# Performance work log

Hardware: AMD Instinct MI355X
Metric: run time of the kernel (lower is better)

## Reference

```python
import jax, jax.numpy as jnp
import numpy as np


def fps(xyz, npoint):
    # xyz: [B, N, 3] -> idx [B, npoint]; iterative farthest point sampling (start at index 0)
    B, N, _ = xyz.shape
    dist0 = jnp.full((B, N), 1e10, xyz.dtype)
    far0 = jnp.zeros((B,), jnp.int32)
    def body(carry, _):
        dist, far = carry
        centroid = jnp.take_along_axis(xyz, far[:, None, None], axis=1)  # [B,1,3]
        d = jnp.sum((xyz - centroid) ** 2, axis=-1)                      # [B,N]
        dist = jnp.minimum(dist, d)
        return (dist, jnp.argmax(dist, axis=-1).astype(jnp.int32)), far
    _, idx = jax.lax.scan(body, (dist0, far0), None, length=npoint)
    return idx.T  # [B, npoint]


def ball_query(radius, nsample, xyz, new_xyz):
    # xyz [B,N,3], new_xyz [B,S,3] -> idx [B,S,nsample]
    B, S, _ = new_xyz.shape
    N = xyz.shape[1]
    sqr = jnp.sum((new_xyz[:, :, None, :] - xyz[:, None, :, :]) ** 2, axis=-1)  # [B,S,N]
    idx = jnp.broadcast_to(jnp.arange(N, dtype=jnp.int32), (B, S, N))
    idx = jnp.where(sqr > radius * radius, N, idx)
    idx = jnp.sort(idx, axis=-1)[:, :, :nsample]
    first = idx[:, :, :1]
    return jnp.where(idx == N, first, idx)


def index_points(points, idx):
    # points [B,N,C], idx [B,...] int -> [B,...,C]
    B = points.shape[0]
    out = jnp.take_along_axis(points, idx.reshape(B, -1, 1), axis=1)
    return out.reshape(idx.shape + (points.shape[-1],))


def set_abstraction(xyz, points, npoint, radius, nsample, ws, bs):
    fidx = fps(xyz, npoint)
    new_xyz = index_points(xyz, fidx)                       # [B,S,3]
    gidx = ball_query(radius, nsample, xyz, new_xyz)        # [B,S,ns]
    grouped = index_points(xyz, gidx) - new_xyz[:, :, None, :]  # centered neighbors
    if points is not None:
        grouped = jnp.concatenate([grouped, index_points(points, gidx)], axis=-1)
    x = grouped                                             # [B,S,ns,Cin]
    for w, b in zip(ws, bs):  # shared 1x1-conv MLP (eval-mode BN folded into w,b) + ReLU
        x = jax.nn.relu(jnp.einsum('bsnc,oc->bsno', x, w) + b)
    return new_xyz, jnp.max(x, axis=2)                      # max-pool over neighbors


def sa_group_all(xyz, points, ws, bs):
    x = jnp.concatenate([xyz, points], axis=-1)             # [B,N,3+C]
    for w, b in zip(ws, bs):
        x = jax.nn.relu(jnp.einsum('bnc,oc->bno', x, w) + b)
    return jnp.max(x, axis=1)                               # [B,1024]


def setup_inputs() -> dict:
    key = jax.random.key(0)
    ks = iter(jax.random.split(key, 64))
    def w(shape):
        return jax.random.normal(next(ks), shape, jnp.float32) * 0.02
    d = {"xyz": jax.random.normal(next(ks), (32, 3, 4096), jnp.float32)}
    mlps = {"s1": [(64, 3), (64, 64), (128, 64)],
            "s2": [(128, 131), (128, 128), (256, 128)],
            "s3": [(256, 259), (512, 256), (1024, 512)]}
    for name, layers in mlps.items():
        for i, (o, c) in enumerate(layers):
            d[name + "w" + str(i)] = w((o, c))
            d[name + "b" + str(i)] = jnp.zeros((o,), jnp.float32)
    for name, (o, c) in {"f1": (512, 1024), "f2": (256, 512), "f3": (6, 256)}.items():
        d[name + "w"] = w((o, c))
        d[name + "b"] = jnp.zeros((o,), jnp.float32)
    return d


def reference(xyz, s1w0, s1b0, s1w1, s1b1, s1w2, s1b2,
              s2w0, s2b0, s2w1, s2b1, s2w2, s2b2,
              s3w0, s3b0, s3w1, s3b1, s3w2, s3b2,
              f1w, f1b, f2w, f2b, f3w, f3b):
    pts = jnp.transpose(xyz, (0, 2, 1))  # [B,N,3]
    l1x, l1p = set_abstraction(pts, None, 512, 0.2, 32, [s1w0, s1w1, s1w2], [s1b0, s1b1, s1b2])
    l2x, l2p = set_abstraction(l1x, l1p, 128, 0.4, 64, [s2w0, s2w1, s2w2], [s2b0, s2b1, s2b2])
    feat = sa_group_all(l2x, l2p, [s3w0, s3w1, s3w2], [s3b0, s3b1, s3b2])  # [B,1024]
    x = jax.nn.relu(feat @ f1w.T + f1b)   # fc1 + (folded BN) + ReLU; dropout=identity (eval)
    x = jax.nn.relu(x @ f2w.T + f2b)
    return x @ f3w.T + f3b                # [B,6] value head (softmax=False)
```

## Files before the change

### kernel.cpp

```cpp
#include <hip/hip_runtime.h>
#include <hip/hip_bf16.h>


typedef __attribute__((ext_vector_type(8))) short short8;
typedef __attribute__((ext_vector_type(4))) float f32x4;
union SV8 { short8 v; ushort u[8]; };

__device__ __forceinline__ ushort f2bf(float x) {
    unsigned u = __float_as_uint(x);
    unsigned r = (u + 0x7fffu + ((u >> 16) & 1u)) >> 16;
    return (ushort)r;
}

template<int CTRL>
__device__ __forceinline__ unsigned long long dpp_mov_u64(unsigned long long x) {
    const int lo = (int)(unsigned)(x & 0xffffffffull);
    const int hi = (int)(unsigned)(x >> 32);
    const int nlo = __builtin_amdgcn_update_dpp(lo, lo, CTRL, 0xf, 0xf, false);
    const int nhi = __builtin_amdgcn_update_dpp(hi, hi, CTRL, 0xf, 0xf, false);
    return ((unsigned long long)(unsigned)nhi << 32) | (unsigned)nlo;
}

__device__ __forceinline__ unsigned long long wave_max_u64(unsigned long long x) {
    unsigned long long y;
    y = dpp_mov_u64<0x111>(x); if (y > x) x = y;
    y = dpp_mov_u64<0x112>(x); if (y > x) x = y;
    y = dpp_mov_u64<0x114>(x); if (y > x) x = y;
    y = dpp_mov_u64<0x118>(x); if (y > x) x = y;
    y = dpp_mov_u64<0x142>(x); if (y > x) x = y;
    y = dpp_mov_u64<0x143>(x); if (y > x) x = y;
    return x;
}

template<int N, int S, int NT, bool CHW>
__device__ __forceinline__ void fps_body(const float* __restrict__ xyz,
                                         float* __restrict__ new_xyz,
                                         int b, int t, char* smem) {
    constexpr int P  = N / NT;
    constexpr int NW = NT / 64;
    float4* sxyz = (float4*)smem;
    unsigned long long* rv = (unsigned long long*)(smem + (size_t)N * 16);
    int* sfar = (int*)(smem + (size_t)N * 16 + 2 * NW * 8);
    float px[P], py[P], pz[P], dist[P];
    unsigned idc[P];
    if (CHW) {
        const float* base = xyz + (size_t)b * 3 * N;
        #pragma unroll
        for (int p = 0; p < P; ++p) {
            const int i = p * NT + t;
            px[p] = base[i]; py[p] = base[N + i]; pz[p] = base[2 * N + i];
            sxyz[i] = make_float4(px[p], py[p], pz[p], 0.0f);
        }
    } else {
        const float* base = xyz + (size_t)b * N * 3;
        #pragma unroll
        for (int p = 0; p < P; ++p) {
            const int i = p * NT + t;
            px[p] = base[i*3]; py[p] = base[i*3+1]; pz[p] = base[i*3+2];
            sxyz[i] = make_float4(px[p], py[p], pz[p], 0.0f);
        }
    }
    #pragma unroll
    for (int p = 0; p < P; ++p) { dist[p] = 1e10f; idc[p] = (unsigned)(N - 1 - (p * NT + t)); }
    __syncthreads();
    int far = 0;
    for (int j = 0; j < S; ++j) {
        if (t == 0) sfar[j] = far;
        const float4 cen = sxyz[far];
        unsigned long long pk[P];
        #pragma unroll
        for (int p = 0; p < P; ++p) {
            const float dx = px[p] - cen.x, dy = py[p] - cen.y, dz = pz[p] - cen.z;
            const float d = __fadd_rn(__fadd_rn(__fmul_rn(dx, dx), __fmul_rn(dy, dy)), __fmul_rn(dz, dz));
            const float nd = fminf(dist[p], d);
            dist[p] = nd;
            pk[p] = ((unsigned long long)__float_as_uint(nd) << 32) | idc[p];
        }
        #pragma unroll
        for (int s = P / 2; s > 0; s >>= 1)
            #pragma unroll
            for (int k = 0; k < s; ++k)
                if (pk[k + s] > pk[k]) pk[k] = pk[k + s];
        unsigned long long best = wave_max_u64(pk[0]);
        if constexpr (NW > 1) {
            const int sl = (j & 1) * NW;
            if ((t & 63) == 63) rv[sl + (t >> 6)] = best;
            __syncthreads();
            unsigned long long bb = rv[sl];
            #pragma unroll
            for (int w = 1; w < NW; ++w) { const unsigned long long v = rv[sl + w]; if (v > bb) bb = v; }
            far = N - 1 - (int)(bb & 0xffffffffull);
        } else {
            far = N - 1 - __builtin_amdgcn_readlane((int)(best & 0xffffffffull), 63);
        }
    }
    __syncthreads();
    float* out = new_xyz + (size_t)b * S * 3;
    for (int i = t; i < S; i += NT) {
        const float4 c = sxyz[sfar[i]];
        out[i*3+0] = c.x; out[i*3+1] = c.y; out[i*3+2] = c.z;
    }
}

__device__ __forceinline__ void packg(const float* __restrict__ src,
                                      ushort* __restrict__ dh,
                                      int Ktot, int otiles, int cofs, int idx) {
    const int j = idx & 7, lane = (idx >> 3) & 63;
    const int ot = (idx >> 9) % otiles;
    const int ks = idx / (512 * otiles);
    const int m = lane & 15, q = lane >> 4;
    const int o = ot * 16 + m, c = cofs + ks * 32 + q * 8 + j;
    const float v = (c < Ktot) ? src[(size_t)o * Ktot + c] : 0.0f;
    dh[idx] = f2bf(v);
}

__global__ __launch_bounds__(256)
void fps1_prep_kernel(const float* __restrict__ xyz, float* __restrict__ l1xyz,
                 const float* s1w0, const float* s1b0, float4* Wc1,
                 const float* s1w1, ushort* M1W1h,
                 const float* s1w2, ushort* M1W2h,
                 const float* s3w0, ushort* S3W0h,
                 const float* s3w1, ushort* S3W1h,
                 const float* s3w2, ushort* S3W2h,
                 const float* s2w0, const float* s2b0, float4* Wc0,
                 ushort* W0h,
                 const float* s2w1, ushort* W1h,
                 const float* s2w2, ushort* W2h) {
    __shared__ __align__(16) char smem[4096 * 16 + 64 + 512 * 4];
    if (blockIdx.x < 32) {
        fps_body<4096, 512, 256, true>(xyz, l1xyz, blockIdx.x, threadIdx.x, smem);
        return;
    }
    int i = (blockIdx.x - 32) * 256 + threadIdx.x;
    if (i < 64)     { Wc1[i] = make_float4(s1w0[i*3], s1w0[i*3+1], s1w0[i*3+2], s1b0[i]); return; }  i -= 64;
    if (i < 4096)   { packg(s1w1, M1W1h,  64,  4, 0, i); return; }   i -= 4096;
    if (i < 8192)   { packg(s1w2, M1W2h,  64,  8, 0, i); return; }   i -= 8192;
    if (i < 73728)  { packg(s3w0, S3W0h, 259, 16, 0, i); return; }   i -= 73728;
    if (i < 131072) { packg(s3w1, S3W1h, 256, 32, 0, i); return; }   i -= 131072;
    if (i < 524288) { packg(s3w2, S3W2h, 512, 64, 0, i); return; }   i -= 524288;
    if (i < 16384)  { packg(s2w0, W0h, 131,  8, 3, i); return; }     i -= 16384;
    if (i < 16384)  { packg(s2w1, W1h, 128,  8, 0, i); return; }     i -= 16384;
    if (i < 32768)  { packg(s2w2, W2h, 128, 16, 0, i); return; }     i -= 32768;
    if (i < 128) {
        Wc0[i] = make_float4(s2w0[(size_t)i*131+0], s2w0[(size_t)i*131+1],
                             s2w0[(size_t)i*131+2], s2b0[i]);
    }
}

template<int N, int NS, bool CHW, int NT>
__global__ __launch_bounds__(NT)
void bq_kernel(float r2, const float* __restrict__ xyz, const float* __restrict__ cen,
               int* __restrict__ gidx, int S) {
    constexpr int WPB = NT / 64;
    __shared__ __align__(16) float4 sp[N];
    const int t = threadIdx.x, lane = t & 63, w = t >> 6;
    const int cen0 = blockIdx.x * WPB;
    const int b = cen0 / S;
    if (CHW) {
        const float* base = xyz + (size_t)b * 3 * N;
        for (int i = t; i < N; i += NT)
            sp[i] = make_float4(base[i], base[N + i], base[2 * N + i], 0.0f);
    } else {
        const float* base = xyz + (size_t)b * N * 3;
        for (int i = t; i < N; i += NT)
            sp[i] = make_float4(base[i*3], base[i*3+1], base[i*3+2], 0.0f);
    }
    __syncthreads();
    const int wid = cen0 + w;
    const float cx = cen[(size_t)wid*3+0], cy = cen[(size_t)wid*3+1], cz = cen[(size_t)wid*3+2];
    int* out = gidx + (size_t)wid * NS;
    int cnt = 0, first = -1;
    for (int b0 = 0; b0 < N; b0 += 64) {
        const float4 p = sp[b0 + lane];
        const float dx = p.x - cx, dy = p.y - cy, dz = p.z - cz;
        const float d = __fadd_rn(__fadd_rn(__fmul_rn(dx, dx), __fmul_rn(dy, dy)), __fmul_rn(dz, dz));
        const bool in = (d <= r2);
        const unsigned long long m = __ballot(in);
        if (first < 0 && m != 0ull) first = b0 + __ffsll((unsigned long long)m) - 1;
        const int pos = cnt + (int)__popcll(m & ((1ull << lane) - 1ull));
        if (in && pos < NS) out[pos] = b0 + lane;
        cnt += (int)__popcll(m);
        if (cnt >= NS) break;
    }
    if (cnt < NS)
        for (int k = cnt + lane; k < NS; k += 64) out[k] = first;
}

__global__ __launch_bounds__(256)
void mlp1_kernel(const float* __restrict__ xyz, const float* __restrict__ l1xyz,
                 float* __restrict__ l2xyz,
                 const int* __restrict__ gidx, const float4* __restrict__ Wc1,
                 const ushort* __restrict__ W1h, const float* __restrict__ b1,
                 const ushort* __restrict__ W2h, const float* __restrict__ b2,
                 float* __restrict__ l1p) {
    __shared__ __align__(16) char smem[64 * 68 * 4 * 2];
    float* bufA = (float*)smem;
    float* bufB = (float*)(smem + 64 * 68 * 4);
    const int t = threadIdx.x, b = blockIdx.y;
    if (blockIdx.x == 256) {
        fps_body<512, 128, 256, false>(l1xyz, l2xyz, b, t, smem);
        return;
    }
    const int s0 = blockIdx.x * 2;
    {
        const int n = t >> 2, c = t & 3;
        const int s = s0 + (n >> 5);
        const int gi = gidx[((size_t)b * 512 + s) * 32 + (n & 31)];
        float v = 0.0f;
        if (c < 3) v = xyz[(size_t)b * 3 * 4096 + c * 4096 + gi] - l1xyz[((size_t)b * 512 + s) * 3 + c];
        bufB[n * 4 + c] = v;
    }
    __syncthreads();
    {
        const int o = t & 63, ng = t >> 6;
        const float4 wc = Wc1[o];
        #pragma unroll
        for (int r = 0; r < 16; ++r) {
            const int n = ng * 16 + r;
            const float z = wc.w + wc.x * bufB[n*4] + wc.y * bufB[n*4+1] + wc.z * bufB[n*4+2];
            bufA[n * 68 + o] = fmaxf(z, 0.0f);
        }
    }
    const int lane = t & 63, wv = t >> 6;
    const int m = lane & 15, q = lane >> 4;
    const int rowA = wv * 16 + m;
    f32x4 acc1[4];
    #pragma unroll
    for (int ot = 0; ot < 4; ++ot)
        #pragma unroll
        for (int r = 0; r < 4; ++r) acc1[ot][r] = 0.0f;
    #pragma unroll
    for (int ks = 0; ks < 2; ++ks) {
        float xv[8];
        *(float4*)&xv[0] = *(const float4*)&bufA[rowA * 68 + ks * 32 + q * 8];
        *(float4*)&xv[4] = *(const float4*)&bufA[rowA * 68 + ks * 32 + q * 8 + 4];
        SV8 ah;
        #pragma unroll
        for (int j = 0; j < 8; ++j) ah.u[j] = f2bf(xv[j]);
        #pragma unroll
        for (int ot = 0; ot < 4; ++ot) {
            SV8 bh;
            bh.v = *(const short8*)(W1h + (size_t)((ks * 4 + ot) * 64 + lane) * 8);
            acc1[ot] = __builtin_amdgcn_mfma_f32_16x16x32_bf16(ah.v, bh.v, acc1[ot], 0, 0, 0);
        }
    }
    #pragma unroll
    for (int ot = 0; ot < 4; ++ot) {
        const float bb = b1[ot * 16 + m];
        #pragma unroll
        for (int r = 0; r < 4; ++r)
            bufB[(wv * 16 + q * 4 + r) * 68 + ot * 16 + m] = fmaxf(acc1[ot][r] + bb, 0.0f);
    }
    f32x4 acc2[8];
    #pragma unroll
    for (int ot = 0; ot < 8; ++ot)
        #pragma unroll
        for (int r = 0; r < 4; ++r) acc2[ot][r] = 0.0f;
    #pragma unroll
    for (int ks = 0; ks < 2; ++ks) {
        float xv[8];
        *(float4*)&xv[0] = *(const float4*)&bufB[rowA * 68 + ks * 32 + q * 8];
        *(float4*)&xv[4] = *(const float4*)&bufB[rowA * 68 + ks * 32 + q * 8 + 4];
        SV8 ah;
        #pragma unroll
        for (int j = 0; j < 8; ++j) ah.u[j] = f2bf(xv[j]);
        #pragma unroll
        for (int ot = 0; ot < 8; ++ot) {
            SV8 bh;
            bh.v = *(const short8*)(W2h + (size_t)((ks * 8 + ot) * 64 + lane) * 8);
            acc2[ot] = __builtin_amdgcn_mfma_f32_16x16x32_bf16(ah.v, bh.v, acc2[ot], 0, 0, 0);
        }
    }
    __syncthreads();
    #pragma unroll
    for (int ot = 0; ot < 8; ++ot) {
        const float bb = b2[ot * 16 + m];
        float mx = 0.0f;
        #pragma unroll
        for (int r = 0; r < 4; ++r) mx = fmaxf(mx, acc2[ot][r] + bb);
        bufA[(wv * 4 + q) * 128 + ot * 16 + m] = mx;
    }
    __syncthreads();
    {
        const int half = t >> 7, o = t & 127;
        float v = bufA[(half * 8) * 128 + o];
        #pragma unroll
        for (int rr = 1; rr < 8; ++rr) v = fmaxf(v, bufA[(half * 8 + rr) * 128 + o]);
        l1p[((size_t)b * 512 + s0 + half) * 128 + o] = v;
    }
}

__global__ __launch_bounds__(256)
void mlp2_kernel(const float* __restrict__ l1xyz, const float* __restrict__ l1p,
                 const float* __restrict__ l2xyz, const int* __restrict__ gidx,
                 const ushort* __restrict__ W0h, const float4* __restrict__ Wc0,
                 const ushort* __restrict__ W1h, const float* __restrict__ b1,
                 const ushort* __restrict__ W2h, const float* __restrict__ b2,
                 float* __restrict__ X3) {
    __shared__ __align__(16) float Abuf[64 * 132];
    __shared__ __align__(16) float Bbuf[64 * 132];
    __shared__ int sg[64];
    const int t = threadIdx.x, bs = blockIdx.x, b = bs >> 7;
    if (t < 64) sg[t] = gidx[(size_t)bs * 64 + t];
    if (t < 3)  X3[(size_t)bs * 288 + t] = l2xyz[(size_t)bs * 3 + t];
    if (t >= 64 && t < 93) X3[(size_t)bs * 288 + 259 + (t - 64)] = 0.0f;
    __syncthreads();
    for (int i = t; i < 64 * 32; i += 256) {
        const int n = i >> 5, cc = i & 31;
        *(float4*)&Abuf[n * 132 + cc * 4] =
            *(const float4*)&l1p[((size_t)b * 512 + sg[n]) * 128 + cc * 4];
    }
    if (t < 192) {
        const int n = t / 3, c = t % 3;
        Abuf[n * 132 + 128 + c] =
            l1xyz[((size_t)b * 512 + sg[n]) * 3 + c] - l2xyz[(size_t)bs * 3 + c];
    }
    __syncthreads();
    const int lane = t & 63, wv = t >> 6;
    const int m = lane & 15, q = lane >> 4;
    const int rowA = wv * 16 + m;

    f32x4 acc0[8];
    #pragma unroll
    for (int ot = 0; ot < 8; ++ot)
        #pragma unroll
        for (int r = 0; r < 4; ++r) acc0[ot][r] = 0.0f;
    #pragma unroll
    for (int ks = 0; ks < 4; ++ks) {
        float xv[8];
        *(float4*)&xv[0] = *(const float4*)&Abuf[rowA * 132 + ks * 32 + q * 8];
        *(float4*)&xv[4] = *(const float4*)&Abuf[rowA * 132 + ks * 32 + q * 8 + 4];
        SV8 ah;
        #pragma unroll
        for (int j = 0; j < 8; ++j) ah.u[j] = f2bf(xv[j]);
        #pragma unroll
        for (int ot = 0; ot < 8; ++ot) {
            SV8 bh;
            bh.v = *(const short8*)(W0h + (size_t)((ks * 8 + ot) * 64 + lane) * 8);
            acc0[ot] = __builtin_amdgcn_mfma_f32_16x16x32_bf16(ah.v, bh.v, acc0[ot], 0, 0, 0);
        }
    }
    float crd[4][3];
    #pragma unroll
    for (int r = 0; r < 4; ++r) {
        const int n = wv * 16 + q * 4 + r;
        crd[r][0] = Abuf[n * 132 + 128];
        crd[r][1] = Abuf[n * 132 + 129];
        crd[r][2] = Abuf[n * 132 + 130];
    }
    #pragma unroll
    for (int ot = 0; ot < 8; ++ot) {
        const float4 wc = Wc0[ot * 16 + m];
        #pragma unroll
        for (int r = 0; r < 4; ++r) {
            const float v = acc0[ot][r] + wc.w + wc.x * crd[r][0] + wc.y * crd[r][1] + wc.z * crd[r][2];
            Bbuf[(wv * 16 + q * 4 + r) * 132 + ot * 16 + m] = fmaxf(v, 0.0f);
        }
    }
    __syncthreads();

    f32x4 acc1[8];
    #pragma unroll
    for (int ot = 0; ot < 8; ++ot)
        #pragma unroll
        for (int r = 0; r < 4; ++r) acc1[ot][r] = 0.0f;
    #pragma unroll
    for (int ks = 0; ks < 4; ++ks) {
        float xv[8];
        *(float4*)&xv[0] = *(const float4*)&Bbuf[rowA * 132 + ks * 32 + q * 8];
        *(float4*)&xv[4] = *(const float4*)&Bbuf[rowA * 132 + ks * 32 + q * 8 + 4];
        SV8 ah;
        #pragma unroll
        for (int j = 0; j < 8; ++j) ah.u[j] = f2bf(xv[j]);
        #pragma unroll
        for (int ot = 0; ot < 8; ++ot) {
            SV8 bh;
            bh.v = *(const short8*)(W1h + (size_t)((ks * 8 + ot) * 64 + lane) * 8);
            acc1[ot] = __builtin_amdgcn_mfma_f32_16x16x32_bf16(ah.v, bh.v, acc1[ot], 0, 0, 0);
        }
    }
    __syncthreads();
    #pragma unroll
    for (int ot = 0; ot < 8; ++ot) {
        const float bb = b1[ot * 16 + m];
        #pragma unroll
        for (int r = 0; r < 4; ++r)
            Abuf[(wv * 16 + q * 4 + r) * 132 + ot * 16 + m] = fmaxf(acc1[ot][r] + bb, 0.0f);
    }
    __syncthreads();

    f32x4 acc2[16];
    #pragma unroll
    for (int ot = 0; ot < 16; ++ot)
        #pragma unroll
        for (int r = 0; r < 4; ++r) acc2[ot][r] = 0.0f;
    #pragma unroll
    for (int ks = 0; ks < 4; ++ks) {
        float xv[8];
        *(float4*)&xv[0] = *(const float4*)&Abuf[rowA * 132 + ks * 32 + q * 8];
        *(float4*)&xv[4] = *(const float4*)&Abuf[rowA * 132 + ks * 32 + q * 8 + 4];
        SV8 ah;
        #pragma unroll
        for (int j = 0; j < 8; ++j) ah.u[j] = f2bf(xv[j]);
        #pragma unroll
        for (int ot = 0; ot < 16; ++ot) {
            SV8 bh;
            bh.v = *(const short8*)(W2h + (size_t)((ks * 16 + ot) * 64 + lane) * 8);
            acc2[ot] = __builtin_amdgcn_mfma_f32_16x16x32_bf16(ah.v, bh.v, acc2[ot], 0, 0, 0);
        }
    }
    __syncthreads();
    #pragma unroll
    for (int ot = 0; ot < 16; ++ot) {
        const float bb = b2[ot * 16 + m];
        float mx = 0.0f;
        #pragma unroll
        for (int r = 0; r < 4; ++r) mx = fmaxf(mx, acc2[ot][r] + bb);
        Bbuf[(wv * 4 + q) * 256 + ot * 16 + m] = mx;
    }
    __syncthreads();
    {
        float v = Bbuf[t];
        #pragma unroll
        for (int rr = 1; rr < 16; ++rr) v = fmaxf(v, Bbuf[rr * 256 + t]);
        X3[(size_t)bs * 288 + 3 + t] = v;
    }
}

template<int KSTEPS, bool MAXOUT>
__global__ __launch_bounds__(256)
void gemm_mfma_kernel(const float* __restrict__ A, int AS,
                      const ushort* __restrict__ Wh,
                      const float* __restrict__ bias, float* __restrict__ C, int O) {
    __shared__ float part[16][64];
    const int t = threadIdx.x, lane = t & 63, wv = t >> 6;
    const int m = lane & 15, q = lane >> 4;
    const int rowA = blockIdx.x * 64 + wv * 16 + m;
    const int bo = blockIdx.y, OT = O >> 4;
    f32x4 acc[4];
    #pragma unroll
    for (int ot = 0; ot < 4; ++ot)
        #pragma unroll
        for (int r = 0; r < 4; ++r) acc[ot][r] = 0.0f;
    for (int ks = 0; ks < KSTEPS; ++ks) {
        float xv[8];
        *(float4*)&xv[0] = *(const float4*)&A[(size_t)rowA * AS + ks * 32 + q * 8];
        *(float4*)&xv[4] = *(const float4*)&A[(size_t)rowA * AS + ks * 32 + q * 8 + 4];
        SV8 ah;
        #pragma unroll
        for (int j = 0; j < 8; ++j) ah.u[j] = f2bf(xv[j]);
        #pragma unroll
        for (int ot = 0; ot < 4; ++ot) {
            const size_t wb = (size_t)((ks * OT + bo * 4 + ot) * 64 + lane) * 8;
            SV8 bh;
            bh.v = *(const short8*)(Wh + wb);
            acc[ot] = __builtin_amdgcn_mfma_f32_16x16x32_bf16(ah.v, bh.v, acc[ot], 0, 0, 0);
        }
    }
    if (!MAXOUT) {
        #pragma unroll
        for (int ot = 0; ot < 4; ++ot) {
            const int col = (bo * 4 + ot) * 16 + m;
            const float bb = bias[col];
            #pragma unroll
            for (int r = 0; r < 4; ++r) {
                const int row = blockIdx.x * 64 + wv * 16 + q * 4 + r;
                C[(size_t)row * O + col] = fmaxf(acc[ot][r] + bb, 0.0f);
            }
        }
    } else {
        #pragma unroll
        for (int ot = 0; ot < 4; ++ot) {
            const int col = (bo * 4 + ot) * 16 + m;
            const float bb = bias[col];
            float mx = 0.0f;
            #pragma unroll
            for (int r = 0; r < 4; ++r) mx = fmaxf(mx, acc[ot][r] + bb);
            part[wv * 4 + q][ot * 16 + m] = mx;
        }
        __syncthreads();
        if (t < 64) {
            float v = part[0][t];
            #pragma unroll
            for (int rr = 1; rr < 16; ++rr) v = fmaxf(v, part[rr][t]);
            C[(size_t)blockIdx.x * O + bo * 64 + t] = v;
        }
    }
}

__global__ __launch_bounds__(256)
void fchead_kernel(const float* __restrict__ P3,
                   const float* __restrict__ f1w, const float* __restrict__ f1b,
                   const float* __restrict__ f2w, const float* __restrict__ f2b,
                   const float* __restrict__ f3w, const float* __restrict__ f3b,
                   float* __restrict__ out) {
    __shared__ __align__(16) float x[1024];
    __shared__ __align__(16) float h1[512];
    __shared__ __align__(16) float h2[256];
    const int t = threadIdx.x, b = blockIdx.x;
    for (int i = t; i < 1024; i += 256)
        x[i] = fmaxf(P3[(size_t)(2*b)*1024 + i], P3[(size_t)(2*b+1)*1024 + i]);
    __syncthreads();
    #pragma unroll
    for (int oo = 0; oo < 2; ++oo) {
        const int o = t + oo * 256;
        const float4* wr = (const float4*)(f1w + (size_t)o * 1024);
        float s0 = 0, s1 = 0, s2 = 0, s3 = 0;
        for (int c = 0; c < 256; ++c) {
            const float4 w4 = wr[c];
            const float4 xv = *(const float4*)&x[c * 4];
            s0 += w4.x * xv.x; s1 += w4.y * xv.y; s2 += w4.z * xv.z; s3 += w4.w * xv.w;
        }
        h1[o] = fmaxf(f1b[o] + ((s0 + s1) + (s2 + s3)), 0.0f);
    }
    __syncthreads();
    {
        const float4* wr = (const float4*)(f2w + (size_t)t * 512);
        float s0 = 0, s1 = 0, s2 = 0, s3 = 0;
        for (int c = 0; c < 128; ++c) {
            const float4 w4 = wr[c];
            const float4 xv = *(const float4*)&h1[c * 4];
            s0 += w4.x * xv.x; s1 += w4.y * xv.y; s2 += w4.z * xv.z; s3 += w4.w * xv.w;
        }
        h2[t] = fmaxf(f2b[t] + ((s0 + s1) + (s2 + s3)), 0.0f);
    }
    __syncthreads();
    if (t < 6) {
        const float4* wr = (const float4*)(f3w + (size_t)t * 256);
        float s0 = 0, s1 = 0, s2 = 0, s3 = 0;
        for (int c = 0; c < 64; ++c) {
            const float4 w4 = wr[c];
            const float4 xv = *(const float4*)&h2[c * 4];
            s0 += w4.x * xv.x; s1 += w4.y * xv.y; s2 += w4.z * xv.z; s3 += w4.w * xv.w;
        }
        out[b * 6 + t] = f3b[t] + ((s0 + s1) + (s2 + s3));
    }
}

extern "C" void kernel_launch(void* const* d_in, const int* in_sizes, int n_in,
                              void* d_out, int out_size, void* d_ws, size_t ws_size,
                              hipStream_t stream) {
    const float* xyz  = (const float*)d_in[0];
    const float* s1w0 = (const float*)d_in[1];  const float* s1b0 = (const float*)d_in[2];
    const float* s1w1 = (const float*)d_in[3];  const float* s1b1 = (const float*)d_in[4];
    const float* s1w2 = (const float*)d_in[5];  const float* s1b2 = (const float*)d_in[6];
    const float* s2w0 = (const float*)d_in[7];  const float* s2b0 = (const float*)d_in[8];
    const float* s2w1 = (const float*)d_in[9];  const float* s2b1 = (const float*)d_in[10];
    const float* s2w2 = (const float*)d_in[11]; const float* s2b2 = (const float*)d_in[12];
    const float* s3w0 = (const float*)d_in[13]; const float* s3b0 = (const float*)d_in[14];
    const float* s3w1 = (const float*)d_in[15]; const float* s3b1 = (const float*)d_in[16];
    const float* s3w2 = (const float*)d_in[17]; const float* s3b2 = (const float*)d_in[18];
    const float* f1w  = (const float*)d_in[19]; const float* f1b  = (const float*)d_in[20];
    const float* f2w  = (const float*)d_in[21]; const float* f2b  = (const float*)d_in[22];
    const float* f3w  = (const float*)d_in[23]; const float* f3b  = (const float*)d_in[24];

    char* ws = (char*)d_ws;
    float* l1_xyz = (float*)(ws + 0);
    int*   gidx1  = (int*)  (ws + 196608);
    float* l1p    = (float*)(ws + 2293760);
    float* l2_xyz = (float*)(ws + 10682368);
    int*   gidx2  = (int*)  (ws + 10731520);
    float* X3p    = (float*)(ws + 11780096);
    const size_t PK = 16498688;
    float4* Wc1   = (float4*)(ws + PK + 0);
    ushort* M1W1h = (ushort*)(ws + PK + 1024);
    ushort* M1W2h = (ushort*)(ws + PK + 17408);
    ushort* W0h   = (ushort*)(ws + PK + 50176);
    ushort* W1h   = (ushort*)(ws + PK + 115712);
    ushort* W2h   = (ushort*)(ws + PK + 181248);
    float4* Wc0   = (float4*)(ws + PK + 312320);
    ushort* S3W0h = (ushort*)(ws + PK + 314368);
    ushort* S3W1h = (ushort*)(ws + PK + 609280);
    ushort* S3W2h = (ushort*)(ws + PK + 1133568);
    float* Y1   = (float*)(ws + 19729408);
    float* Y2   = (float*)(ws + 23923712);
    float* P3   = (float*)(ws + 32312320);

    fps1_prep_kernel<<<3186, 256, 0, stream>>>(xyz, l1_xyz,
        s1w0, s1b0, Wc1, s1w1, M1W1h, s1w2, M1W2h,
        s3w0, S3W0h, s3w1, S3W1h, s3w2, S3W2h,
        s2w0, s2b0, Wc0, W0h, s2w1, W1h, s2w2, W2h);
    bq_kernel<4096, 32, true, 1024><<<1024, 1024, 0, stream>>>(
        (float)(0.2 * 0.2), xyz, l1_xyz, gidx1, 512);
    {
        dim3 g(257, 32);
        mlp1_kernel<<<g, 256, 0, stream>>>(xyz, l1_xyz, l2_xyz, gidx1,
            Wc1, M1W1h, s1b1, M1W2h, s1b2, l1p);
    }

    bq_kernel<512, 64, false, 1024><<<256, 1024, 0, stream>>>(
        (float)(0.4 * 0.4), l1_xyz, l2_xyz, gidx2, 128);
    mlp2_kernel<<<4096, 256, 0, stream>>>(l1_xyz, l1p, l2_xyz, gidx2,
        W0h, Wc0, W1h, s2b1, W2h, s2b2, X3p);

    {
        dim3 g1(64, 4);
        gemm_mfma_kernel<9,  false><<<g1, 256, 0, stream>>>(X3p, 288, S3W0h, s3b0, Y1, 256);
        dim3 g2(64, 8);
        gemm_mfma_kernel<8,  false><<<g2, 256, 0, stream>>>(Y1, 256, S3W1h, s3b1, Y2, 512);
        dim3 g3(64, 16);
        gemm_mfma_kernel<16, true ><<<g3, 256, 0, stream>>>(Y2, 512, S3W2h, s3b2, P3, 1024);
    }

    fchead_kernel<<<32, 256, 0, stream>>>(P3, f1w, f1b, f2w, f2b, f3w, f3b, (float*)d_out);
    (void)in_sizes; (void)n_in; (void)out_size; (void)ws_size;
}
```

Before: 783.6 us.

## Store intermediate activations in bf16 across MLP kernels and shared memory

Intermediate activations (l1 features, X3, Y1, Y2) and the shared-memory staging buffers now hold bf16 instead of fp32. The f2bf conversion moves to the producer side, so MFMA operands are loaded straight as short8. This halves global and LDS traffic for activations, removes the repeated per-consumer conversion, and shrinks LDS use, which may allow higher occupancy. It adds rounding at a few new points, such as the max-pooled outputs and the coordinates in X3, which slightly changes numerics.

```diff
diff --git a/kernel.cpp b/kernel.cpp
--- a/kernel.cpp
+++ b/kernel.cpp
@@ -192,15 +192,17 @@
                  const int* __restrict__ gidx, const float4* __restrict__ Wc1,
                  const ushort* __restrict__ W1h, const float* __restrict__ b1,
                  const ushort* __restrict__ W2h, const float* __restrict__ b2,
-                 float* __restrict__ l1p) {
-    __shared__ __align__(16) char smem[64 * 68 * 4 * 2];
-    float* bufA = (float*)smem;
-    float* bufB = (float*)(smem + 64 * 68 * 4);
+                 ushort* __restrict__ l1p) {
+    __shared__ __align__(16) char smem[20480];
     const int t = threadIdx.x, b = blockIdx.y;
     if (blockIdx.x == 256) {
         fps_body<512, 128, 256, false>(l1xyz, l2xyz, b, t, smem);
         return;
     }
+    float*  g  = (float*)smem;
+    ushort* hA = (ushort*)(smem + 1024);
+    ushort* hB = (ushort*)(smem + 1024 + 9216);
+    float*  red = (float*)(smem + 1024);
     const int s0 = blockIdx.x * 2;
     {
         const int n = t >> 2, c = t & 3;
@@ -208,7 +210,7 @@
         const int gi = gidx[((size_t)b * 512 + s) * 32 + (n & 31)];
         float v = 0.0f;
         if (c < 3) v = xyz[(size_t)b * 3 * 4096 + c * 4096 + gi] - l1xyz[((size_t)b * 512 + s) * 3 + c];
-        bufB[n * 4 + c] = v;
+        g[n * 4 + c] = v;
     }
     __syncthreads();
     {
@@ -217,8 +219,8 @@
         #pragma unroll
         for (int r = 0; r < 16; ++r) {
             const int n = ng * 16 + r;
-            const float z = wc.w + wc.x * bufB[n*4] + wc.y * bufB[n*4+1] + wc.z * bufB[n*4+2];
-            bufA[n * 68 + o] = fmaxf(z, 0.0f);
+            const float z = wc.w + wc.x * g[n*4] + wc.y * g[n*4+1] + wc.z * g[n*4+2];
+            hA[n * 72 + o] = f2bf(fmaxf(z, 0.0f));
         }
     }
     const int lane = t & 63, wv = t >> 6;
@@ -231,17 +233,11 @@
         for (int r = 0; r < 4; ++r) acc1[ot][r] = 0.0f;
     #pragma unroll
     for (int ks = 0; ks < 2; ++ks) {
-        float xv[8];
-        *(float4*)&xv[0] = *(const float4*)&bufA[rowA * 68 + ks * 32 + q * 8];
-        *(float4*)&xv[4] = *(const float4*)&bufA[rowA * 68 + ks * 32 + q * 8 + 4];
-        SV8 ah;
-        #pragma unroll
-        for (int j = 0; j < 8; ++j) ah.u[j] = f2bf(xv[j]);
+        const short8 av = *(const short8*)&hA[rowA * 72 + ks * 32 + q * 8];
         #pragma unroll
         for (int ot = 0; ot < 4; ++ot) {
-            SV8 bh;
-            bh.v = *(const short8*)(W1h + (size_t)((ks * 4 + ot) * 64 + lane) * 8);
-            acc1[ot] = __builtin_amdgcn_mfma_f32_16x16x32_bf16(ah.v, bh.v, acc1[ot], 0, 0, 0);
+            const short8 bv = *(const short8*)(W1h + (size_t)((ks * 4 + ot) * 64 + lane) * 8);
+            acc1[ot] = __builtin_amdgcn_mfma_f32_16x16x32_bf16(av, bv, acc1[ot], 0, 0, 0);
         }
     }
     #pragma unroll
@@ -249,7 +245,7 @@
         const float bb = b1[ot * 16 + m];
         #pragma unroll
         for (int r = 0; r < 4; ++r)
-            bufB[(wv * 16 + q * 4 + r) * 68 + ot * 16 + m] = fmaxf(acc1[ot][r] + bb, 0.0f);
+            hB[(wv * 16 + q * 4 + r) * 72 + ot * 16 + m] = f2bf(fmaxf(acc1[ot][r] + bb, 0.0f));
     }
     f32x4 acc2[8];
     #pragma unroll
@@ -258,17 +254,11 @@
         for (int r = 0; r < 4; ++r) acc2[ot][r] = 0.0f;
     #pragma unroll
     for (int ks = 0; ks < 2; ++ks) {
-        float xv[8];
-        *(float4*)&xv[0] = *(const float4*)&bufB[rowA * 68 + ks * 32 + q * 8];
-        *(float4*)&xv[4] = *(const float4*)&bufB[rowA * 68 + ks * 32 + q * 8 + 4];
-        SV8 ah;
-        #pragma unroll
-        for (int j = 0; j < 8; ++j) ah.u[j] = f2bf(xv[j]);
+        const short8 av = *(const short8*)&hB[rowA * 72 + ks * 32 + q * 8];
         #pragma unroll
         for (int ot = 0; ot < 8; ++ot) {
-            SV8 bh;
-            bh.v = *(const short8*)(W2h + (size_t)((ks * 8 + ot) * 64 + lane) * 8);
-            acc2[ot] = __builtin_amdgcn_mfma_f32_16x16x32_bf16(ah.v, bh.v, acc2[ot], 0, 0, 0);
+            const short8 bv = *(const short8*)(W2h + (size_t)((ks * 8 + ot) * 64 + lane) * 8);
+            acc2[ot] = __builtin_amdgcn_mfma_f32_16x16x32_bf16(av, bv, acc2[ot], 0, 0, 0);
         }
     }
     __syncthreads();
@@ -278,42 +268,43 @@
         float mx = 0.0f;
         #pragma unroll
         for (int r = 0; r < 4; ++r) mx = fmaxf(mx, acc2[ot][r] + bb);
-        bufA[(wv * 4 + q) * 128 + ot * 16 + m] = mx;
+        red[(wv * 4 + q) * 128 + ot * 16 + m] = mx;
     }
     __syncthreads();
     {
         const int half = t >> 7, o = t & 127;
-        float v = bufA[(half * 8) * 128 + o];
-        #pragma unroll
-        for (int rr = 1; rr < 8; ++rr) v = fmaxf(v, bufA[(half * 8 + rr) * 128 + o]);
-        l1p[((size_t)b * 512 + s0 + half) * 128 + o] = v;
+        float v = red[(half * 8) * 128 + o];
+        #pragma unroll
+        for (int rr = 1; rr < 8; ++rr) v = fmaxf(v, red[(half * 8 + rr) * 128 + o]);
+        l1p[((size_t)b * 512 + s0 + half) * 128 + o] = f2bf(v);
     }
 }
 
 __global__ __launch_bounds__(256)
-void mlp2_kernel(const float* __restrict__ l1xyz, const float* __restrict__ l1p,
+void mlp2_kernel(const float* __restrict__ l1xyz, const ushort* __restrict__ l1p,
                  const float* __restrict__ l2xyz, const int* __restrict__ gidx,
                  const ushort* __restrict__ W0h, const float4* __restrict__ Wc0,
                  const ushort* __restrict__ W1h, const float* __restrict__ b1,
                  const ushort* __restrict__ W2h, const float* __restrict__ b2,
-                 float* __restrict__ X3) {
-    __shared__ __align__(16) float Abuf[64 * 132];
-    __shared__ __align__(16) float Bbuf[64 * 132];
+                 ushort* __restrict__ X3) {
     __shared__ int sg[64];
+    __shared__ __align__(16) float crd[64 * 4];
+    __shared__ __align__(16) ushort Abuf[64 * 136];
+    __shared__ __align__(16) ushort Bbuf[64 * 136];
+    float* Bf = (float*)Bbuf;
     const int t = threadIdx.x, bs = blockIdx.x, b = bs >> 7;
     if (t < 64) sg[t] = gidx[(size_t)bs * 64 + t];
-    if (t < 3)  X3[(size_t)bs * 288 + t] = l2xyz[(size_t)bs * 3 + t];
-    if (t >= 64 && t < 93) X3[(size_t)bs * 288 + 259 + (t - 64)] = 0.0f;
-    __syncthreads();
-    for (int i = t; i < 64 * 32; i += 256) {
-        const int n = i >> 5, cc = i & 31;
-        *(float4*)&Abuf[n * 132 + cc * 4] =
-            *(const float4*)&l1p[((size_t)b * 512 + sg[n]) * 128 + cc * 4];
+    if (t < 3)  X3[(size_t)bs * 288 + t] = f2bf(l2xyz[(size_t)bs * 3 + t]);
+    if (t >= 64 && t < 93) X3[(size_t)bs * 288 + 259 + (t - 64)] = 0;
+    __syncthreads();
+    for (int i = t; i < 64 * 16; i += 256) {
+        const int n = i >> 4, cc = i & 15;
+        *(uint4*)&Abuf[n * 136 + cc * 8] =
+            *(const uint4*)&l1p[((size_t)b * 512 + sg[n]) * 128 + cc * 8];
     }
     if (t < 192) {
         const int n = t / 3, c = t % 3;
-        Abuf[n * 132 + 128 + c] =
-            l1xyz[((size_t)b * 512 + sg[n]) * 3 + c] - l2xyz[(size_t)bs * 3 + c];
+        crd[n * 4 + c] = l1xyz[((size_t)b * 512 + sg[n]) * 3 + c] - l2xyz[(size_t)bs * 3 + c];
     }
     __syncthreads();
     const int lane = t & 63, wv = t >> 6;
@@ -327,34 +318,26 @@
         for (int r = 0; r < 4; ++r) acc0[ot][r] = 0.0f;
     #pragma unroll
     for (int ks = 0; ks < 4; ++ks) {
-        float xv[8];
-        *(float4*)&xv[0] = *(const float4*)&Abuf[rowA * 132 + ks * 32 + q * 8];
-        *(float4*)&xv[4] = *(const float4*)&Abuf[rowA * 132 + ks * 32 + q * 8 + 4];
-        SV8 ah;
-        #pragma unroll
-        for (int j = 0; j < 8; ++j) ah.u[j] = f2bf(xv[j]);
+        const short8 av = *(const short8*)&Abuf[rowA * 136 + ks * 32 + q * 8];
         #pragma unroll
         for (int ot = 0; ot < 8; ++ot) {
-            SV8 bh;
-            bh.v = *(const short8*)(W0h + (size_t)((ks * 8 + ot) * 64 + lane) * 8);
-            acc0[ot] = __builtin_amdgcn_mfma_f32_16x16x32_bf16(ah.v, bh.v, acc0[ot], 0, 0, 0);
-        }
-    }
-    float crd[4][3];
+            const short8 bv = *(const short8*)(W0h + (size_t)((ks * 8 + ot) * 64 + lane) * 8);
+            acc0[ot] = __builtin_amdgcn_mfma_f32_16x16x32_bf16(av, bv, acc0[ot], 0, 0, 0);
+        }
+    }
+    float cr[4][3];
     #pragma unroll
     for (int r = 0; r < 4; ++r) {
         const int n = wv * 16 + q * 4 + r;
-        crd[r][0] = Abuf[n * 132 + 128];
-        crd[r][1] = Abuf[n * 132 + 129];
-        crd[r][2] = Abuf[n * 132 + 130];
+        cr[r][0] = crd[n * 4 + 0]; cr[r][1] = crd[n * 4 + 1]; cr[r][2] = crd[n * 4 + 2];
     }
     #pragma unroll
     for (int ot = 0; ot < 8; ++ot) {
         const float4 wc = Wc0[ot * 16 + m];
         #pragma unroll
         for (int r = 0; r < 4; ++r) {
-            const float v = acc0[ot][r] + wc.w + wc.x * crd[r][0] + wc.y * crd[r][1] + wc.z * crd[r][2];
-            Bbuf[(wv * 16 + q * 4 + r) * 132 + ot * 16 + m] = fmaxf(v, 0.0f);
+            const float v = acc0[ot][r] + wc.w + wc.x * cr[r][0] + wc.y * cr[r][1] + wc.z * cr[r][2];
+            Bbuf[(wv * 16 + q * 4 + r) * 136 + ot * 16 + m] = f2bf(fmaxf(v, 0.0f));
         }
     }
     __syncthreads();
@@ -366,17 +349,11 @@
         for (int r = 0; r < 4; ++r) acc1[ot][r] = 0.0f;
     #pragma unroll
     for (int ks = 0; ks < 4; ++ks) {
-        float xv[8];
-        *(float4*)&xv[0] = *(const float4*)&Bbuf[rowA * 132 + ks * 32 + q * 8];
-        *(float4*)&xv[4] = *(const float4*)&Bbuf[rowA * 132 + ks * 32 + q * 8 + 4];
-        SV8 ah;
-        #pragma unroll
-        for (int j = 0; j < 8; ++j) ah.u[j] = f2bf(xv[j]);
+        const short8 av = *(const short8*)&Bbuf[rowA * 136 + ks * 32 + q * 8];
         #pragma unroll
         for (int ot = 0; ot < 8; ++ot) {
-            SV8 bh;
-            bh.v = *(const short8*)(W1h + (size_t)((ks * 8 + ot) * 64 + lane) * 8);
-            acc1[ot] = __builtin_amdgcn_mfma_f32_16x16x32_bf16(ah.v, bh.v, acc1[ot], 0, 0, 0);
+            const short8 bv = *(const short8*)(W1h + (size_t)((ks * 8 + ot) * 64 + lane) * 8);
+            acc1[ot] = __builtin_amdgcn_mfma_f32_16x16x32_bf16(av, bv, acc1[ot], 0, 0, 0);
         }
     }
     __syncthreads();
@@ -385,7 +362,7 @@
         const float bb = b1[ot * 16 + m];
         #pragma unroll
         for (int r = 0; r < 4; ++r)
-            Abuf[(wv * 16 + q * 4 + r) * 132 + ot * 16 + m] = fmaxf(acc1[ot][r] + bb, 0.0f);
+            Abuf[(wv * 16 + q * 4 + r) * 136 + ot * 16 + m] = f2bf(fmaxf(acc1[ot][r] + bb, 0.0f));
     }
     __syncthreads();
 
@@ -396,17 +373,11 @@
         for (int r = 0; r < 4; ++r) acc2[ot][r] = 0.0f;
     #pragma unroll
     for (int ks = 0; ks < 4; ++ks) {
-        float xv[8];
-        *(float4*)&xv[0] = *(const float4*)&Abuf[rowA * 132 + ks * 32 + q * 8];
-        *(float4*)&xv[4] = *(const float4*)&Abuf[rowA * 132 + ks * 32 + q * 8 + 4];
-        SV8 ah;
-        #pragma unroll
-        for (int j = 0; j < 8; ++j) ah.u[j] = f2bf(xv[j]);
+        const short8 av = *(const short8*)&Abuf[rowA * 136 + ks * 32 + q * 8];
         #pragma unroll
         for (int ot = 0; ot < 16; ++ot) {
-            SV8 bh;
-            bh.v = *(const short8*)(W2h + (size_t)((ks * 16 + ot) * 64 + lane) * 8);
-            acc2[ot] = __builtin_amdgcn_mfma_f32_16x16x32_bf16(ah.v, bh.v, acc2[ot], 0, 0, 0);
+            const short8 bv = *(const short8*)(W2h + (size_t)((ks * 16 + ot) * 64 + lane) * 8);
+            acc2[ot] = __builtin_amdgcn_mfma_f32_16x16x32_bf16(av, bv, acc2[ot], 0, 0, 0);
         }
     }
     __syncthreads();
@@ -416,22 +387,22 @@
         float mx = 0.0f;
         #pragma unroll
         for (int r = 0; r < 4; ++r) mx = fmaxf(mx, acc2[ot][r] + bb);
-        Bbuf[(wv * 4 + q) * 256 + ot * 16 + m] = mx;
-    }
-    __syncthreads();
-    {
-        float v = Bbuf[t];
-        #pragma unroll
-        for (int rr = 1; rr < 16; ++rr) v = fmaxf(v, Bbuf[rr * 256 + t]);
-        X3[(size_t)bs * 288 + 3 + t] = v;
+        Bf[(wv * 4 + q) * 256 + ot * 16 + m] = mx;
+    }
+    __syncthreads();
+    {
+        float v = Bf[t];
+        #pragma unroll
+        for (int rr = 1; rr < 16; ++rr) v = fmaxf(v, Bf[rr * 256 + t]);
+        X3[(size_t)bs * 288 + 3 + t] = f2bf(v);
     }
 }
 
 template<int KSTEPS, bool MAXOUT>
 __global__ __launch_bounds__(256)
-void gemm_mfma_kernel(const float* __restrict__ A, int AS,
+void gemm_mfma_kernel(const ushort* __restrict__ A, int AS,
                       const ushort* __restrict__ Wh,
-                      const float* __restrict__ bias, float* __restrict__ C, int O) {
+                      const float* __restrict__ bias, void* __restrict__ Cv, int O) {
     __shared__ float part[16][64];
     const int t = threadIdx.x, lane = t & 63, wv = t >> 6;
     const int m = lane & 15, q = lane >> 4;
@@ -443,21 +414,15 @@
         #pragma unroll
         for (int r = 0; r < 4; ++r) acc[ot][r] = 0.0f;
     for (int ks = 0; ks < KSTEPS; ++ks) {
-        float xv[8];
-        *(float4*)&xv[0] = *(const float4*)&A[(size_t)rowA * AS + ks * 32 + q * 8];
-        *(float4*)&xv[4] = *(const float4*)&A[(size_t)rowA * AS + ks * 32 + q * 8 + 4];
-        SV8 ah;
-        #pragma unroll
-        for (int j = 0; j < 8; ++j) ah.u[j] = f2bf(xv[j]);
+        const short8 av = *(const short8*)&A[(size_t)rowA * AS + ks * 32 + q * 8];
         #pragma unroll
         for (int ot = 0; ot < 4; ++ot) {
-            const size_t wb = (size_t)((ks * OT + bo * 4 + ot) * 64 + lane) * 8;
-            SV8 bh;
-            bh.v = *(const short8*)(Wh + wb);
-            acc[ot] = __builtin_amdgcn_mfma_f32_16x16x32_bf16(ah.v, bh.v, acc[ot], 0, 0, 0);
+            const short8 bv = *(const short8*)(Wh + (size_t)((ks * OT + bo * 4 + ot) * 64 + lane) * 8);
+            acc[ot] = __builtin_amdgcn_mfma_f32_16x16x32_bf16(av, bv, acc[ot], 0, 0, 0);
         }
     }
     if (!MAXOUT) {
+        ushort* C = (ushort*)Cv;
         #pragma unroll
         for (int ot = 0; ot < 4; ++ot) {
             const int col = (bo * 4 + ot) * 16 + m;
@@ -465,10 +430,11 @@
             #pragma unroll
             for (int r = 0; r < 4; ++r) {
                 const int row = blockIdx.x * 64 + wv * 16 + q * 4 + r;
-                C[(size_t)row * O + col] = fmaxf(acc[ot][r] + bb, 0.0f);
+                C[(size_t)row * O + col] = f2bf(fmaxf(acc[ot][r] + bb, 0.0f));
             }
         }
     } else {
+        float* C = (float*)Cv;
         #pragma unroll
         for (int ot = 0; ot < 4; ++ot) {
             const int col = (bo * 4 + ot) * 16 + m;
@@ -555,13 +521,13 @@
     const float* f3w  = (const float*)d_in[23]; const float* f3b  = (const float*)d_in[24];
 
     char* ws = (char*)d_ws;
-    float* l1_xyz = (float*)(ws + 0);
-    int*   gidx1  = (int*)  (ws + 196608);
-    float* l1p    = (float*)(ws + 2293760);
-    float* l2_xyz = (float*)(ws + 10682368);
-    int*   gidx2  = (int*)  (ws + 10731520);
-    float* X3p    = (float*)(ws + 11780096);
-    const size_t PK = 16498688;
+    float*  l1_xyz = (float*) (ws + 0);
+    int*    gidx1  = (int*)   (ws + 196608);
+    ushort* l1p    = (ushort*)(ws + 2293760);
+    float*  l2_xyz = (float*) (ws + 6488064);
+    int*    gidx2  = (int*)   (ws + 6537216);
+    ushort* X3p    = (ushort*)(ws + 7585792);
+    const size_t PK = 9945088;
     float4* Wc1   = (float4*)(ws + PK + 0);
     ushort* M1W1h = (ushort*)(ws + PK + 1024);
     ushort* M1W2h = (ushort*)(ws + PK + 17408);
@@ -572,9 +538,9 @@
     ushort* S3W0h = (ushort*)(ws + PK + 314368);
     ushort* S3W1h = (ushort*)(ws + PK + 609280);
     ushort* S3W2h = (ushort*)(ws + PK + 1133568);
-    float* Y1   = (float*)(ws + 19729408);
-    float* Y2   = (float*)(ws + 23923712);
-    float* P3   = (float*)(ws + 32312320);
+    ushort* Y1 = (ushort*)(ws + 12127232);
+    ushort* Y2 = (ushort*)(ws + 14224384);
+    float*  P3 = (float*) (ws + 18418688);
 
     fps1_prep_kernel<<<3186, 256, 0, stream>>>(xyz, l1_xyz,
         s1w0, s1b0, Wc1, s1w1, M1W1h, s1w2, M1W2h,
```

New measurement: 837.4 us. 6.9% more time.
